# Kernel tuning notes

Hardware: AMD Instinct MI355X
Metric: run time of the kernel (lower is better)

Reference implementation:

```python
import jax, jax.numpy as jnp
import numpy as np

T, B, DIM, LATENT, OUT = 512, 1024, 128, 256, 64


def setup_inputs() -> dict:
    key = jax.random.key(0)
    ks = jax.random.split(key, 6)
    s_i = 1.0 / np.sqrt(DIM)
    s_h = 1.0 / np.sqrt(LATENT)
    return {
        "x": jax.random.normal(ks[0], (T, B, DIM), dtype=jnp.float32),
        "h": jnp.zeros((B, LATENT), dtype=jnp.float32),
        "Wi": jax.random.uniform(ks[1], (DIM, LATENT), jnp.float32, -s_i, s_i),
        "bi": jax.random.uniform(ks[2], (LATENT,), jnp.float32, -s_i, s_i),
        "Wh": jax.random.uniform(ks[3], (LATENT, LATENT), jnp.float32, -s_h, s_h),
        "Wd": jax.random.uniform(ks[4], (LATENT, OUT), jnp.float32, -s_h, s_h),
        "bd": jax.random.uniform(ks[5], (OUT,), jnp.float32, -s_h, s_h),
    }


def reference(x, h, Wi, bi, Wh, Wd, bd):
    # Precompute input projections for all steps in one big GEMM: [T,B,latent]
    xi = jnp.einsum("tbd,dl->tbl", x, Wi) + bi

    def step(h, xi_t):
        h = jnp.tanh(xi_t + h @ Wh)
        return h, None

    h_final, _ = jax.lax.scan(step, h, xi)
    return jax.nn.sigmoid(h_final @ Wd + bd)
```

## Files before the change

### kernel.cpp

```cpp
#include <hip/hip_runtime.h>
#include <cmath>
#include <cstdint>

constexpr int T_STEPS = 512;
constexpr int BATCH   = 1024;
constexpr int DIM     = 128;
constexpr int LATENT  = 256;
constexpr int OUT_DIM = 64;
constexpr int ROWS    = 16;

typedef __attribute__((ext_vector_type(8))) short bf16x8;
typedef __attribute__((ext_vector_type(4))) float f32x4;
typedef __attribute__((ext_vector_type(4))) int   i32x4;

__device__ __forceinline__ uint32_t f2bf(float f) {
    uint32_t u = __builtin_bit_cast(uint32_t, f);
    return (u + 0x7FFFu + ((u >> 16) & 1u)) >> 16;
}
__device__ __forceinline__ uint32_t pk2(float a, float b) {
    return f2bf(a) | (f2bf(b) << 16);
}
__device__ __forceinline__ float fast_tanh(float v) {
    float e = __builtin_amdgcn_exp2f(v * 2.885390081777927f);
    return __builtin_fmaf(-2.0f, __builtin_amdgcn_rcpf(e + 1.0f), 1.0f);
}
__device__ __forceinline__ float fast_sigmoid(float v) {
    float e = __builtin_amdgcn_exp2f(v * -1.4426950408889634f);
    return __builtin_amdgcn_rcpf(e + 1.0f);
}
__device__ __forceinline__ int q8(float v, float inv) {
    return (int)__builtin_rintf(v * inv);
}
__device__ __forceinline__ uint32_t pack4(int a, int b, int c, int d) {
    return (uint32_t)(a & 255) | ((uint32_t)(b & 255) << 8) |
           ((uint32_t)(c & 255) << 16) | ((uint32_t)(d & 255) << 24);
}
__device__ __forceinline__ int swz(int sl, int b) {
    return (sl ^ (b & 3) ^ ((b >> 2) & 3)) & 3;
}

__global__ __launch_bounds__(512)
void rnn_i8h(const float* __restrict__ x,
             const float* __restrict__ h0,
             const float* __restrict__ Wi,
             const float* __restrict__ bi,
             const float* __restrict__ Wh,
             const float* __restrict__ Wd,
             const float* __restrict__ bd,
             float* __restrict__ out)
{
    __shared__ __align__(16) uint8_t hls[2][4096];
    __shared__ __align__(16) uint8_t xls[2][4096];

    const int tid  = threadIdx.x;
    const int lane = tid & 63;
    const int wv   = tid >> 6;
    const int b0   = blockIdx.x * ROWS;
    const int b15  = lane & 15;
    const int kgrp = lane >> 4;
    const int tg0  = wv * 2, tg1 = wv * 2 + 1;
    const int wcol0 = tg0 * 16 + b15;
    const int wcol1 = wcol0 + 16;

    float cmh0 = 0.f, cmh1 = 0.f;
    {
        const float* p0 = Wh + (size_t)(kgrp * 16) * LATENT + wcol0;
        #pragma unroll 4
        for (int i = 0; i < 64; ++i) {
            const size_t off = (size_t)((i >> 4) * 64 + (i & 15)) * LATENT;
            cmh0 = fmaxf(cmh0, fabsf(p0[off]));
            cmh1 = fmaxf(cmh1, fabsf(p0[off + 16]));
        }
        cmh0 = fmaxf(cmh0, __shfl_xor(cmh0, 16));
        cmh0 = fmaxf(cmh0, __shfl_xor(cmh0, 32));
        cmh1 = fmaxf(cmh1, __shfl_xor(cmh1, 16));
        cmh1 = fmaxf(cmh1, __shfl_xor(cmh1, 32));
    }
    const float ih0 = cmh0 > 0.f ? 127.f / cmh0 : 0.f;
    const float ih1 = cmh1 > 0.f ? 127.f / cmh1 : 0.f;

#define WHQ(J) q8(_p[(size_t)(J) * LATENT], _inv)
#define LOADWH(NAME, WC, S, INV)                                            \
    i32x4 NAME; {                                                           \
        const float* _p = Wh + (size_t)((S) * 64 + kgrp * 16) * LATENT + (WC); \
        const float _inv = (INV);                                           \
        NAME[0] = (int)pack4(WHQ(0),  WHQ(1),  WHQ(2),  WHQ(3));            \
        NAME[1] = (int)pack4(WHQ(4),  WHQ(5),  WHQ(6),  WHQ(7));            \
        NAME[2] = (int)pack4(WHQ(8),  WHQ(9),  WHQ(10), WHQ(11));           \
        NAME[3] = (int)pack4(WHQ(12), WHQ(13), WHQ(14), WHQ(15));           \
    }
    LOADWH(AH0_0, wcol0, 0, ih0) LOADWH(AH0_1, wcol0, 1, ih0)
    LOADWH(AH0_2, wcol0, 2, ih0) LOADWH(AH0_3, wcol0, 3, ih0)
    LOADWH(AH1_0, wcol1, 0, ih1) LOADWH(AH1_1, wcol1, 1, ih1)
    LOADWH(AH1_2, wcol1, 2, ih1) LOADWH(AH1_3, wcol1, 3, ih1)

#define LOADWX(NAME, WC, S)                                                 \
    bf16x8 NAME; {                                                          \
        const float* _p = Wi + (size_t)((S) * 32 + kgrp * 8) * LATENT + (WC); \
        NAME[0] = (short)f2bf(_p[0]);                                       \
        NAME[1] = (short)f2bf(_p[(size_t)1 * LATENT]);                      \
        NAME[2] = (short)f2bf(_p[(size_t)2 * LATENT]);                      \
        NAME[3] = (short)f2bf(_p[(size_t)3 * LATENT]);                      \
        NAME[4] = (short)f2bf(_p[(size_t)4 * LATENT]);                      \
        NAME[5] = (short)f2bf(_p[(size_t)5 * LATENT]);                      \
        NAME[6] = (short)f2bf(_p[(size_t)6 * LATENT]);                      \
        NAME[7] = (short)f2bf(_p[(size_t)7 * LATENT]);                      \
    }
    LOADWX(AX0_0, wcol0, 0) LOADWX(AX0_1, wcol0, 1)
    LOADWX(AX0_2, wcol0, 2) LOADWX(AX0_3, wcol0, 3)
    LOADWX(AX1_0, wcol1, 0) LOADWX(AX1_1, wcol1, 1)
    LOADWX(AX1_2, wcol1, 2) LOADWX(AX1_3, wcol1, 3)

    const float dh0_0 = __shfl(cmh0, kgrp * 4 + 0) * (1.f / 16129.f);
    const float dh0_1 = __shfl(cmh0, kgrp * 4 + 1) * (1.f / 16129.f);
    const float dh0_2 = __shfl(cmh0, kgrp * 4 + 2) * (1.f / 16129.f);
    const float dh0_3 = __shfl(cmh0, kgrp * 4 + 3) * (1.f / 16129.f);
    const float dh1_0 = __shfl(cmh1, kgrp * 4 + 0) * (1.f / 16129.f);
    const float dh1_1 = __shfl(cmh1, kgrp * 4 + 1) * (1.f / 16129.f);
    const float dh1_2 = __shfl(cmh1, kgrp * 4 + 2) * (1.f / 16129.f);
    const float dh1_3 = __shfl(cmh1, kgrp * 4 + 3) * (1.f / 16129.f);
    const float cb0_0 = bi[tg0 * 16 + kgrp * 4 + 0];
    const float cb0_1 = bi[tg0 * 16 + kgrp * 4 + 1];
    const float cb0_2 = bi[tg0 * 16 + kgrp * 4 + 2];
    const float cb0_3 = bi[tg0 * 16 + kgrp * 4 + 3];
    const float cb1_0 = bi[tg1 * 16 + kgrp * 4 + 0];
    const float cb1_1 = bi[tg1 * 16 + kgrp * 4 + 1];
    const float cb1_2 = bi[tg1 * 16 + kgrp * 4 + 2];
    const float cb1_3 = bi[tg1 * 16 + kgrp * 4 + 3];

    const int pr = tid & 15;
    const int pq = tid >> 4;
    const int stb = (pq >> 3) * 1024 + pr * 64 +
                    (swz((pq >> 1) & 3, pr) << 4) + (pq & 1) * 8;
    {
        const float* hp = h0 + (size_t)(b0 + pr) * LATENT + pq * 8;
        uint32_t u0 = pack4(q8(hp[0], 127.f), q8(hp[1], 127.f),
                            q8(hp[2], 127.f), q8(hp[3], 127.f));
        uint32_t u1 = pack4(q8(hp[4], 127.f), q8(hp[5], 127.f),
                            q8(hp[6], 127.f), q8(hp[7], 127.f));
        *reinterpret_cast<uint2*>(&hls[0][stb]) = make_uint2(u0, u1);
        const float* xq = x + (size_t)(b0 + pr) * DIM + pq * 4;
        float4 xv = *reinterpret_cast<const float4*>(xq);
        *reinterpret_cast<uint2*>(&xls[0][stb]) =
            make_uint2(pk2(xv.x, xv.y), pk2(xv.z, xv.w));
    }
    __syncthreads();

    const int hrd = b15 * 64 + (swz(kgrp, b15) << 4);
    const int wb0 = (tg0 >> 2) * 1024 + b15 * 64 +
                    (swz(tg0 & 3, b15) << 4) + kgrp * 4;
    const int wb1 = (tg1 >> 2) * 1024 + b15 * 64 +
                    (swz(tg1 & 3, b15) << 4) + kgrp * 4;
    const float* xp = x + ((size_t)BATCH + b0 + pr) * DIM + pq * 4;

    int cur = 0;
    for (int t = 0; t < T_STEPS; ++t) {
        const bool pf = (t + 1 < T_STEPS);
        float4 xv;
        if (pf) {
            xv = *reinterpret_cast<const float4*>(xp);
            xp += (size_t)BATCH * DIM;
        }

        const uint8_t* hb = &hls[cur][hrd];
        const uint8_t* xb = &xls[cur][hrd];
        i32x4  bh0 = *reinterpret_cast<const i32x4*>(hb);
        i32x4  bh1 = *reinterpret_cast<const i32x4*>(hb + 1024);
        i32x4  bh2 = *reinterpret_cast<const i32x4*>(hb + 2048);
        i32x4  bh3 = *reinterpret_cast<const i32x4*>(hb + 3072);
        bf16x8 bx0 = *reinterpret_cast<const bf16x8*>(xb);
        bf16x8 bx1 = *reinterpret_cast<const bf16x8*>(xb + 1024);
        bf16x8 bx2 = *reinterpret_cast<const bf16x8*>(xb + 2048);
        bf16x8 bx3 = *reinterpret_cast<const bf16x8*>(xb + 3072);

        i32x4 ch0 = {0, 0, 0, 0}, ch1 = {0, 0, 0, 0};
        f32x4 cx0 = {cb0_0, cb0_1, cb0_2, cb0_3};
        f32x4 cx1 = {cb1_0, cb1_1, cb1_2, cb1_3};

        ch0 = __builtin_amdgcn_mfma_i32_16x16x64_i8(AH0_0, bh0, ch0, 0, 0, 0);
        ch1 = __builtin_amdgcn_mfma_i32_16x16x64_i8(AH1_0, bh0, ch1, 0, 0, 0);
        cx0 = __builtin_amdgcn_mfma_f32_16x16x32_bf16(AX0_0, bx0, cx0, 0, 0, 0);
        cx1 = __builtin_amdgcn_mfma_f32_16x16x32_bf16(AX1_0, bx0, cx1, 0, 0, 0);
        ch0 = __builtin_amdgcn_mfma_i32_16x16x64_i8(AH0_1, bh1, ch0, 0, 0, 0);
        ch1 = __builtin_amdgcn_mfma_i32_16x16x64_i8(AH1_1, bh1, ch1, 0, 0, 0);
        cx0 = __builtin_amdgcn_mfma_f32_16x16x32_bf16(AX0_1, bx1, cx0, 0, 0, 0);
        cx1 = __builtin_amdgcn_mfma_f32_16x16x32_bf16(AX1_1, bx1, cx1, 0, 0, 0);
        ch0 = __builtin_amdgcn_mfma_i32_16x16x64_i8(AH0_2, bh2, ch0, 0, 0, 0);
        ch1 = __builtin_amdgcn_mfma_i32_16x16x64_i8(AH1_2, bh2, ch1, 0, 0, 0);
        cx0 = __builtin_amdgcn_mfma_f32_16x16x32_bf16(AX0_2, bx2, cx0, 0, 0, 0);
        cx1 = __builtin_amdgcn_mfma_f32_16x16x32_bf16(AX1_2, bx2, cx1, 0, 0, 0);
        ch0 = __builtin_amdgcn_mfma_i32_16x16x64_i8(AH0_3, bh3, ch0, 0, 0, 0);
        ch1 = __builtin_amdgcn_mfma_i32_16x16x64_i8(AH1_3, bh3, ch1, 0, 0, 0);
        cx0 = __builtin_amdgcn_mfma_f32_16x16x32_bf16(AX0_3, bx3, cx0, 0, 0, 0);
        cx1 = __builtin_amdgcn_mfma_f32_16x16x32_bf16(AX1_3, bx3, cx1, 0, 0, 0);

        const int nxt = cur ^ 1;
        {
            float v0 = fast_tanh(__builtin_fmaf((float)ch0[0], dh0_0, cx0[0]));
            float v1 = fast_tanh(__builtin_fmaf((float)ch0[1], dh0_1, cx0[1]));
            float v2 = fast_tanh(__builtin_fmaf((float)ch0[2], dh0_2, cx0[2]));
            float v3 = fast_tanh(__builtin_fmaf((float)ch0[3], dh0_3, cx0[3]));
            *reinterpret_cast<uint32_t*>(&hls[nxt][wb0]) =
                pack4(q8(v0, 127.f), q8(v1, 127.f), q8(v2, 127.f), q8(v3, 127.f));
        }
        {
            float v0 = fast_tanh(__builtin_fmaf((float)ch1[0], dh1_0, cx1[0]));
            float v1 = fast_tanh(__builtin_fmaf((float)ch1[1], dh1_1, cx1[1]));
            float v2 = fast_tanh(__builtin_fmaf((float)ch1[2], dh1_2, cx1[2]));
            float v3 = fast_tanh(__builtin_fmaf((float)ch1[3], dh1_3, cx1[3]));
            *reinterpret_cast<uint32_t*>(&hls[nxt][wb1]) =
                pack4(q8(v0, 127.f), q8(v1, 127.f), q8(v2, 127.f), q8(v3, 127.f));
        }
        if (pf)
            *reinterpret_cast<uint2*>(&xls[nxt][stb]) =
                make_uint2(pk2(xv.x, xv.y), pk2(xv.z, xv.w));

        __syncthreads();
        cur = nxt;
    }

    {
        const int o  = tid & 63;
        const int rb = tid >> 6;
        float s0 = 0.f, s1 = 0.f;
        #pragma unroll 4
        for (int k = 0; k < LATENT; k += 4) {
            const int sl   = (k >> 4) & 3;
            const int base = (k >> 6) * 1024 + (k & 15);
            const uint32_t pA = *reinterpret_cast<const uint32_t*>(
                &hls[cur][base + rb * 64 + (swz(sl, rb) << 4)]);
            const uint32_t pB = *reinterpret_cast<const uint32_t*>(
                &hls[cur][base + (rb + 8) * 64 + (swz(sl, rb + 8) << 4)]);
            const float w0 = Wd[(size_t)(k + 0) * OUT_DIM + o];
            const float w1 = Wd[(size_t)(k + 1) * OUT_DIM + o];
            const float w2 = Wd[(size_t)(k + 2) * OUT_DIM + o];
            const float w3 = Wd[(size_t)(k + 3) * OUT_DIM + o];
            s0 += (float)(int8_t)(pA) * w0 + (float)(int8_t)(pA >> 8) * w1
                + (float)(int8_t)(pA >> 16) * w2 + (float)(int8_t)(pA >> 24) * w3;
            s1 += (float)(int8_t)(pB) * w0 + (float)(int8_t)(pB >> 8) * w1
                + (float)(int8_t)(pB >> 16) * w2 + (float)(int8_t)(pB >> 24) * w3;
        }
        out[(size_t)(b0 + rb) * OUT_DIM + o] =
            fast_sigmoid(bd[o] + s0 * (1.f / 127.f));
        out[(size_t)(b0 + rb + 8) * OUT_DIM + o] =
            fast_sigmoid(bd[o] + s1 * (1.f / 127.f));
    }
}

extern "C" void kernel_launch(void* const* d_in, const int* in_sizes, int n_in,
                              void* d_out, int out_size, void* d_ws, size_t ws_size,
                              hipStream_t stream) {
    const float* x  = (const float*)d_in[0];
    const float* h0 = (const float*)d_in[1];
    const float* Wi = (const float*)d_in[2];
    const float* bi = (const float*)d_in[3];
    const float* Wh = (const float*)d_in[4];
    const float* Wd = (const float*)d_in[5];
    const float* bd = (const float*)d_in[6];
    float* out = (float*)d_out;

    hipLaunchKernelGGL(rnn_i8h, dim3(BATCH / ROWS), dim3(512), 0, stream,
                       x, h0, Wi, bi, Wh, Wd, bd, out);
}
```

Baseline: 402.8 us.

## Split input projection into a parallel GEMM kernel ahead of recurrence

Moves the x·Wi input projection out of the sequential recurrent loop into a separate kernel that is parallel over time chunks. It writes bf16 pre-activations to workspace, and the recurrence kernel then only streams them from memory. This takes the bf16 MFMAs and the x conversion off the serial critical path. In exchange it adds a workspace round trip (about 256 MB written and then read) and a second kernel launch, and it keeps the fused kernel as a fallback when workspace is too small.

```diff
diff --git a/kernel.cpp b/kernel.cpp
--- a/kernel.cpp
+++ b/kernel.cpp
@@ -8,6 +8,7 @@
 constexpr int LATENT  = 256;
 constexpr int OUT_DIM = 64;
 constexpr int ROWS    = 16;
+constexpr int TCHUNK  = 64;
 
 typedef __attribute__((ext_vector_type(8))) short bf16x8;
 typedef __attribute__((ext_vector_type(4))) float f32x4;
@@ -17,6 +18,9 @@
     uint32_t u = __builtin_bit_cast(uint32_t, f);
     return (u + 0x7FFFu + ((u >> 16) & 1u)) >> 16;
 }
+__device__ __forceinline__ float bf2f(uint32_t b) {
+    return __builtin_bit_cast(float, b << 16);
+}
 __device__ __forceinline__ uint32_t pk2(float a, float b) {
     return f2bf(a) | (f2bf(b) << 16);
 }
@@ -38,46 +42,6 @@
 __device__ __forceinline__ int swz(int sl, int b) {
     return (sl ^ (b & 3) ^ ((b >> 2) & 3)) & 3;
 }
-
-__global__ __launch_bounds__(512)
-void rnn_i8h(const float* __restrict__ x,
-             const float* __restrict__ h0,
-             const float* __restrict__ Wi,
-             const float* __restrict__ bi,
-             const float* __restrict__ Wh,
-             const float* __restrict__ Wd,
-             const float* __restrict__ bd,
-             float* __restrict__ out)
-{
-    __shared__ __align__(16) uint8_t hls[2][4096];
-    __shared__ __align__(16) uint8_t xls[2][4096];
-
-    const int tid  = threadIdx.x;
-    const int lane = tid & 63;
-    const int wv   = tid >> 6;
-    const int b0   = blockIdx.x * ROWS;
-    const int b15  = lane & 15;
-    const int kgrp = lane >> 4;
-    const int tg0  = wv * 2, tg1 = wv * 2 + 1;
-    const int wcol0 = tg0 * 16 + b15;
-    const int wcol1 = wcol0 + 16;
-
-    float cmh0 = 0.f, cmh1 = 0.f;
-    {
-        const float* p0 = Wh + (size_t)(kgrp * 16) * LATENT + wcol0;
-        #pragma unroll 4
-        for (int i = 0; i < 64; ++i) {
-            const size_t off = (size_t)((i >> 4) * 64 + (i & 15)) * LATENT;
-            cmh0 = fmaxf(cmh0, fabsf(p0[off]));
-            cmh1 = fmaxf(cmh1, fabsf(p0[off + 16]));
-        }
-        cmh0 = fmaxf(cmh0, __shfl_xor(cmh0, 16));
-        cmh0 = fmaxf(cmh0, __shfl_xor(cmh0, 32));
-        cmh1 = fmaxf(cmh1, __shfl_xor(cmh1, 16));
-        cmh1 = fmaxf(cmh1, __shfl_xor(cmh1, 32));
-    }
-    const float ih0 = cmh0 > 0.f ? 127.f / cmh0 : 0.f;
-    const float ih1 = cmh1 > 0.f ? 127.f / cmh1 : 0.f;
 
 #define WHQ(J) q8(_p[(size_t)(J) * LATENT], _inv)
 #define LOADWH(NAME, WC, S, INV)                                            \
@@ -89,11 +53,6 @@
         NAME[2] = (int)pack4(WHQ(8),  WHQ(9),  WHQ(10), WHQ(11));           \
         NAME[3] = (int)pack4(WHQ(12), WHQ(13), WHQ(14), WHQ(15));           \
     }
-    LOADWH(AH0_0, wcol0, 0, ih0) LOADWH(AH0_1, wcol0, 1, ih0)
-    LOADWH(AH0_2, wcol0, 2, ih0) LOADWH(AH0_3, wcol0, 3, ih0)
-    LOADWH(AH1_0, wcol1, 0, ih1) LOADWH(AH1_1, wcol1, 1, ih1)
-    LOADWH(AH1_2, wcol1, 2, ih1) LOADWH(AH1_3, wcol1, 3, ih1)
-
 #define LOADWX(NAME, WC, S)                                                 \
     bf16x8 NAME; {                                                          \
         const float* _p = Wi + (size_t)((S) * 32 + kgrp * 8) * LATENT + (WC); \
@@ -106,10 +65,137 @@
         NAME[6] = (short)f2bf(_p[(size_t)6 * LATENT]);                      \
         NAME[7] = (short)f2bf(_p[(size_t)7 * LATENT]);                      \
     }
+
+__global__ __launch_bounds__(512)
+void rnn_xi_gemm(const float* __restrict__ x,
+                 const float* __restrict__ Wi,
+                 const float* __restrict__ bi,
+                 uint2* __restrict__ xi)
+{
+    __shared__ __align__(16) uint8_t xls[2][4096];
+
+    const int tid  = threadIdx.x;
+    const int lane = tid & 63;
+    const int wv   = tid >> 6;
+    const int blk  = blockIdx.x;
+    const int t0   = blockIdx.y * TCHUNK;
+    const int b0   = blk * ROWS;
+    const int b15  = lane & 15;
+    const int kgrp = lane >> 4;
+    const int tg0  = wv * 2, tg1 = wv * 2 + 1;
+    const int wcol0 = tg0 * 16 + b15;
+    const int wcol1 = wcol0 + 16;
+
     LOADWX(AX0_0, wcol0, 0) LOADWX(AX0_1, wcol0, 1)
     LOADWX(AX0_2, wcol0, 2) LOADWX(AX0_3, wcol0, 3)
     LOADWX(AX1_0, wcol1, 0) LOADWX(AX1_1, wcol1, 1)
     LOADWX(AX1_2, wcol1, 2) LOADWX(AX1_3, wcol1, 3)
+
+    const float cb0_0 = bi[tg0 * 16 + kgrp * 4 + 0];
+    const float cb0_1 = bi[tg0 * 16 + kgrp * 4 + 1];
+    const float cb0_2 = bi[tg0 * 16 + kgrp * 4 + 2];
+    const float cb0_3 = bi[tg0 * 16 + kgrp * 4 + 3];
+    const float cb1_0 = bi[tg1 * 16 + kgrp * 4 + 0];
+    const float cb1_1 = bi[tg1 * 16 + kgrp * 4 + 1];
+    const float cb1_2 = bi[tg1 * 16 + kgrp * 4 + 2];
+    const float cb1_3 = bi[tg1 * 16 + kgrp * 4 + 3];
+
+    const int pr = tid & 15;
+    const int pq = tid >> 4;
+    const int stb = (pq >> 3) * 1024 + pr * 64 +
+                    (swz((pq >> 1) & 3, pr) << 4) + (pq & 1) * 8;
+    {
+        const float* xq = x + ((size_t)t0 * BATCH + b0 + pr) * DIM + pq * 4;
+        float4 xv = *reinterpret_cast<const float4*>(xq);
+        *reinterpret_cast<uint2*>(&xls[0][stb]) =
+            make_uint2(pk2(xv.x, xv.y), pk2(xv.z, xv.w));
+    }
+    __syncthreads();
+
+    const int hrd = b15 * 64 + (swz(kgrp, b15) << 4);
+    const float* xp = x + ((size_t)(t0 + 1) * BATCH + b0 + pr) * DIM + pq * 4;
+    uint2* wp = xi + ((((size_t)t0 * 64 + blk) << 10) + (wv << 7) + lane);
+
+    int cur = 0;
+    for (int tt = 0; tt < TCHUNK; ++tt) {
+        const bool pf = (tt + 1 < TCHUNK);
+        float4 xv;
+        if (pf) {
+            xv = *reinterpret_cast<const float4*>(xp);
+            xp += (size_t)BATCH * DIM;
+        }
+
+        const uint8_t* xb = &xls[cur][hrd];
+        bf16x8 bx0 = *reinterpret_cast<const bf16x8*>(xb);
+        bf16x8 bx1 = *reinterpret_cast<const bf16x8*>(xb + 1024);
+        bf16x8 bx2 = *reinterpret_cast<const bf16x8*>(xb + 2048);
+        bf16x8 bx3 = *reinterpret_cast<const bf16x8*>(xb + 3072);
+
+        f32x4 c0 = {cb0_0, cb0_1, cb0_2, cb0_3};
+        f32x4 c1 = {cb1_0, cb1_1, cb1_2, cb1_3};
+        c0 = __builtin_amdgcn_mfma_f32_16x16x32_bf16(AX0_0, bx0, c0, 0, 0, 0);
+        c1 = __builtin_amdgcn_mfma_f32_16x16x32_bf16(AX1_0, bx0, c1, 0, 0, 0);
+        c0 = __builtin_amdgcn_mfma_f32_16x16x32_bf16(AX0_1, bx1, c0, 0, 0, 0);
+        c1 = __builtin_amdgcn_mfma_f32_16x16x32_bf16(AX1_1, bx1, c1, 0, 0, 0);
+        c0 = __builtin_amdgcn_mfma_f32_16x16x32_bf16(AX0_2, bx2, c0, 0, 0, 0);
+        c1 = __builtin_amdgcn_mfma_f32_16x16x32_bf16(AX1_2, bx2, c1, 0, 0, 0);
+        c0 = __builtin_amdgcn_mfma_f32_16x16x32_bf16(AX0_3, bx3, c0, 0, 0, 0);
+        c1 = __builtin_amdgcn_mfma_f32_16x16x32_bf16(AX1_3, bx3, c1, 0, 0, 0);
+
+        wp[0]  = make_uint2(pk2(c0[0], c0[1]), pk2(c0[2], c0[3]));
+        wp[64] = make_uint2(pk2(c1[0], c1[1]), pk2(c1[2], c1[3]));
+        wp += 65536;
+
+        if (pf)
+            *reinterpret_cast<uint2*>(&xls[cur ^ 1][stb]) =
+                make_uint2(pk2(xv.x, xv.y), pk2(xv.z, xv.w));
+        __syncthreads();
+        cur ^= 1;
+    }
+}
+
+__global__ __launch_bounds__(512)
+void rnn_rec(const float* __restrict__ h0,
+             const float* __restrict__ Wh,
+             const float* __restrict__ Wd,
+             const float* __restrict__ bd,
+             const uint2* __restrict__ xi,
+             float* __restrict__ out)
+{
+    __shared__ __align__(16) uint8_t hls[2][4096];
+
+    const int tid  = threadIdx.x;
+    const int lane = tid & 63;
+    const int wv   = tid >> 6;
+    const int blk  = blockIdx.x;
+    const int b0   = blk * ROWS;
+    const int b15  = lane & 15;
+    const int kgrp = lane >> 4;
+    const int tg0  = wv * 2, tg1 = wv * 2 + 1;
+    const int wcol0 = tg0 * 16 + b15;
+    const int wcol1 = wcol0 + 16;
+
+    float cmh0 = 0.f, cmh1 = 0.f;
+    {
+        const float* p0 = Wh + (size_t)(kgrp * 16) * LATENT + wcol0;
+        #pragma unroll 4
+        for (int i = 0; i < 64; ++i) {
+            const size_t off = (size_t)((i >> 4) * 64 + (i & 15)) * LATENT;
+            cmh0 = fmaxf(cmh0, fabsf(p0[off]));
+            cmh1 = fmaxf(cmh1, fabsf(p0[off + 16]));
+        }
+        cmh0 = fmaxf(cmh0, __shfl_xor(cmh0, 16));
+        cmh0 = fmaxf(cmh0, __shfl_xor(cmh0, 32));
+        cmh1 = fmaxf(cmh1, __shfl_xor(cmh1, 16));
+        cmh1 = fmaxf(cmh1, __shfl_xor(cmh1, 32));
+    }
+    const float ih0 = cmh0 > 0.f ? 127.f / cmh0 : 0.f;
+    const float ih1 = cmh1 > 0.f ? 127.f / cmh1 : 0.f;
+
+    LOADWH(AH0_0, wcol0, 0, ih0) LOADWH(AH0_1, wcol0, 1, ih0)
+    LOADWH(AH0_2, wcol0, 2, ih0) LOADWH(AH0_3, wcol0, 3, ih0)
+    LOADWH(AH1_0, wcol1, 0, ih1) LOADWH(AH1_1, wcol1, 1, ih1)
+    LOADWH(AH1_2, wcol1, 2, ih1) LOADWH(AH1_3, wcol1, 3, ih1)
 
     const float dh0_0 = __shfl(cmh0, kgrp * 4 + 0) * (1.f / 16129.f);
     const float dh0_1 = __shfl(cmh0, kgrp * 4 + 1) * (1.f / 16129.f);
@@ -119,14 +205,6 @@
     const float dh1_1 = __shfl(cmh1, kgrp * 4 + 1) * (1.f / 16129.f);
     const float dh1_2 = __shfl(cmh1, kgrp * 4 + 2) * (1.f / 16129.f);
     const float dh1_3 = __shfl(cmh1, kgrp * 4 + 3) * (1.f / 16129.f);
-    const float cb0_0 = bi[tg0 * 16 + kgrp * 4 + 0];
-    const float cb0_1 = bi[tg0 * 16 + kgrp * 4 + 1];
-    const float cb0_2 = bi[tg0 * 16 + kgrp * 4 + 2];
-    const float cb0_3 = bi[tg0 * 16 + kgrp * 4 + 3];
-    const float cb1_0 = bi[tg1 * 16 + kgrp * 4 + 0];
-    const float cb1_1 = bi[tg1 * 16 + kgrp * 4 + 1];
-    const float cb1_2 = bi[tg1 * 16 + kgrp * 4 + 2];
-    const float cb1_3 = bi[tg1 * 16 + kgrp * 4 + 3];
 
     const int pr = tid & 15;
     const int pq = tid >> 4;
@@ -139,10 +217,6 @@
         uint32_t u1 = pack4(q8(hp[4], 127.f), q8(hp[5], 127.f),
                             q8(hp[6], 127.f), q8(hp[7], 127.f));
         *reinterpret_cast<uint2*>(&hls[0][stb]) = make_uint2(u0, u1);
-        const float* xq = x + (size_t)(b0 + pr) * DIM + pq * 4;
-        float4 xv = *reinterpret_cast<const float4*>(xq);
-        *reinterpret_cast<uint2*>(&xls[0][stb]) =
-            make_uint2(pk2(xv.x, xv.y), pk2(xv.z, xv.w));
     }
     __syncthreads();
 
@@ -151,70 +225,56 @@
                     (swz(tg0 & 3, b15) << 4) + kgrp * 4;
     const int wb1 = (tg1 >> 2) * 1024 + b15 * 64 +
                     (swz(tg1 & 3, b15) << 4) + kgrp * 4;
-    const float* xp = x + ((size_t)BATCH + b0 + pr) * DIM + pq * 4;
+
+    const uint2* xr = xi + ((size_t)blk << 10) + (wv << 7) + lane;
+    uint2 xa0 = xr[0];
+    uint2 xa1 = xr[64];
 
     int cur = 0;
     for (int t = 0; t < T_STEPS; ++t) {
         const bool pf = (t + 1 < T_STEPS);
-        float4 xv;
+        uint2 xb0, xb1;
         if (pf) {
-            xv = *reinterpret_cast<const float4*>(xp);
-            xp += (size_t)BATCH * DIM;
+            xb0 = xr[65536];
+            xb1 = xr[65536 + 64];
         }
 
         const uint8_t* hb = &hls[cur][hrd];
-        const uint8_t* xb = &xls[cur][hrd];
-        i32x4  bh0 = *reinterpret_cast<const i32x4*>(hb);
-        i32x4  bh1 = *reinterpret_cast<const i32x4*>(hb + 1024);
-        i32x4  bh2 = *reinterpret_cast<const i32x4*>(hb + 2048);
-        i32x4  bh3 = *reinterpret_cast<const i32x4*>(hb + 3072);
-        bf16x8 bx0 = *reinterpret_cast<const bf16x8*>(xb);
-        bf16x8 bx1 = *reinterpret_cast<const bf16x8*>(xb + 1024);
-        bf16x8 bx2 = *reinterpret_cast<const bf16x8*>(xb + 2048);
-        bf16x8 bx3 = *reinterpret_cast<const bf16x8*>(xb + 3072);
+        i32x4 bh0 = *reinterpret_cast<const i32x4*>(hb);
+        i32x4 bh1 = *reinterpret_cast<const i32x4*>(hb + 1024);
+        i32x4 bh2 = *reinterpret_cast<const i32x4*>(hb + 2048);
+        i32x4 bh3 = *reinterpret_cast<const i32x4*>(hb + 3072);
 
         i32x4 ch0 = {0, 0, 0, 0}, ch1 = {0, 0, 0, 0};
-        f32x4 cx0 = {cb0_0, cb0_1, cb0_2, cb0_3};
-        f32x4 cx1 = {cb1_0, cb1_1, cb1_2, cb1_3};
-
         ch0 = __builtin_amdgcn_mfma_i32_16x16x64_i8(AH0_0, bh0, ch0, 0, 0, 0);
         ch1 = __builtin_amdgcn_mfma_i32_16x16x64_i8(AH1_0, bh0, ch1, 0, 0, 0);
-        cx0 = __builtin_amdgcn_mfma_f32_16x16x32_bf16(AX0_0, bx0, cx0, 0, 0, 0);
-        cx1 = __builtin_amdgcn_mfma_f32_16x16x32_bf16(AX1_0, bx0, cx1, 0, 0, 0);
         ch0 = __builtin_amdgcn_mfma_i32_16x16x64_i8(AH0_1, bh1, ch0, 0, 0, 0);
         ch1 = __builtin_amdgcn_mfma_i32_16x16x64_i8(AH1_1, bh1, ch1, 0, 0, 0);
-        cx0 = __builtin_amdgcn_mfma_f32_16x16x32_bf16(AX0_1, bx1, cx0, 0, 0, 0);
-        cx1 = __builtin_amdgcn_mfma_f32_16x16x32_bf16(AX1_1, bx1, cx1, 0, 0, 0);
         ch0 = __builtin_amdgcn_mfma_i32_16x16x64_i8(AH0_2, bh2, ch0, 0, 0, 0);
         ch1 = __builtin_amdgcn_mfma_i32_16x16x64_i8(AH1_2, bh2, ch1, 0, 0, 0);
-        cx0 = __builtin_amdgcn_mfma_f32_16x16x32_bf16(AX0_2, bx2, cx0, 0, 0, 0);
-        cx1 = __builtin_amdgcn_mfma_f32_16x16x32_bf16(AX1_2, bx2, cx1, 0, 0, 0);
         ch0 = __builtin_amdgcn_mfma_i32_16x16x64_i8(AH0_3, bh3, ch0, 0, 0, 0);
         ch1 = __builtin_amdgcn_mfma_i32_16x16x64_i8(AH1_3, bh3, ch1, 0, 0, 0);
-        cx0 = __builtin_amdgcn_mfma_f32_16x16x32_bf16(AX0_3, bx3, cx0, 0, 0, 0);
-        cx1 = __builtin_amdgcn_mfma_f32_16x16x32_bf16(AX1_3, bx3, cx1, 0, 0, 0);
 
         const int nxt = cur ^ 1;
         {
-            float v0 = fast_tanh(__builtin_fmaf((float)ch0[0], dh0_0, cx0[0]));
-            float v1 = fast_tanh(__builtin_fmaf((float)ch0[1], dh0_1, cx0[1]));
-            float v2 = fast_tanh(__builtin_fmaf((float)ch0[2], dh0_2, cx0[2]));
-            float v3 = fast_tanh(__builtin_fmaf((float)ch0[3], dh0_3, cx0[3]));
+            float v0 = fast_tanh(__builtin_fmaf((float)ch0[0], dh0_0, bf2f(xa0.x & 0xFFFFu)));
+            float v1 = fast_tanh(__builtin_fmaf((float)ch0[1], dh0_1, bf2f(xa0.x >> 16)));
+            float v2 = fast_tanh(__builtin_fmaf((float)ch0[2], dh0_2, bf2f(xa0.y & 0xFFFFu)));
+            float v3 = fast_tanh(__builtin_fmaf((float)ch0[3], dh0_3, bf2f(xa0.y >> 16)));
             *reinterpret_cast<uint32_t*>(&hls[nxt][wb0]) =
                 pack4(q8(v0, 127.f), q8(v1, 127.f), q8(v2, 127.f), q8(v3, 127.f));
         }
         {
-            float v0 = fast_tanh(__builtin_fmaf((float)ch1[0], dh1_0, cx1[0]));
-            float v1 = fast_tanh(__builtin_fmaf((float)ch1[1], dh1_1, cx1[1]));
-            float v2 = fast_tanh(__builtin_fmaf((float)ch1[2], dh1_2, cx1[2]));
-            float v3 = fast_tanh(__builtin_fmaf((float)ch1[3], dh1_3, cx1[3]));
+            float v0 = fast_tanh(__builtin_fmaf((float)ch1[0], dh1_0, bf2f(xa1.x & 0xFFFFu)));
+            float v1 = fast_tanh(__builtin_fmaf((float)ch1[1], dh1_1, bf2f(xa1.x >> 16)));
+            float v2 = fast_tanh(__builtin_fmaf((float)ch1[2], dh1_2, bf2f(xa1.y & 0xFFFFu)));
+            float v3 = fast_tanh(__builtin_fmaf((float)ch1[3], dh1_3, bf2f(xa1.y >> 16)));
             *reinterpret_cast<uint32_t*>(&hls[nxt][wb1]) =
                 pack4(q8(v0, 127.f), q8(v1, 127.f), q8(v2, 127.f), q8(v3, 127.f));
         }
-        if (pf)
-            *reinterpret_cast<uint2*>(&xls[nxt][stb]) =
-                make_uint2(pk2(xv.x, xv.y), pk2(xv.z, xv.w));
-
+
+        if (pf) { xa0 = xb0; xa1 = xb1; }
+        xr += 65536;
         __syncthreads();
         cur = nxt;
     }
@@ -247,6 +307,184 @@
     }
 }
 
+__global__ __launch_bounds__(512)
+void rnn_i8h(const float* __restrict__ x, const float* __restrict__ h0,
+             const float* __restrict__ Wi, const float* __restrict__ bi,
+             const float* __restrict__ Wh, const float* __restrict__ Wd,
+             const float* __restrict__ bd, float* __restrict__ out)
+{
+    __shared__ __align__(16) uint8_t hls[2][4096];
+    __shared__ __align__(16) uint8_t xls[2][4096];
+
+    const int tid  = threadIdx.x;
+    const int lane = tid & 63;
+    const int wv   = tid >> 6;
+    const int b0   = blockIdx.x * ROWS;
+    const int b15  = lane & 15;
+    const int kgrp = lane >> 4;
+    const int tg0  = wv * 2, tg1 = wv * 2 + 1;
+    const int wcol0 = tg0 * 16 + b15;
+    const int wcol1 = wcol0 + 16;
+
+    float cmh0 = 0.f, cmh1 = 0.f;
+    {
+        const float* p0 = Wh + (size_t)(kgrp * 16) * LATENT + wcol0;
+        #pragma unroll 4
+        for (int i = 0; i < 64; ++i) {
+            const size_t off = (size_t)((i >> 4) * 64 + (i & 15)) * LATENT;
+            cmh0 = fmaxf(cmh0, fabsf(p0[off]));
+            cmh1 = fmaxf(cmh1, fabsf(p0[off + 16]));
+        }
+        cmh0 = fmaxf(cmh0, __shfl_xor(cmh0, 16));
+        cmh0 = fmaxf(cmh0, __shfl_xor(cmh0, 32));
+        cmh1 = fmaxf(cmh1, __shfl_xor(cmh1, 16));
+        cmh1 = fmaxf(cmh1, __shfl_xor(cmh1, 32));
+    }
+    const float ih0 = cmh0 > 0.f ? 127.f / cmh0 : 0.f;
+    const float ih1 = cmh1 > 0.f ? 127.f / cmh1 : 0.f;
+
+    LOADWH(FH0_0, wcol0, 0, ih0) LOADWH(FH0_1, wcol0, 1, ih0)
+    LOADWH(FH0_2, wcol0, 2, ih0) LOADWH(FH0_3, wcol0, 3, ih0)
+    LOADWH(FH1_0, wcol1, 0, ih1) LOADWH(FH1_1, wcol1, 1, ih1)
+    LOADWH(FH1_2, wcol1, 2, ih1) LOADWH(FH1_3, wcol1, 3, ih1)
+    LOADWX(FX0_0, wcol0, 0) LOADWX(FX0_1, wcol0, 1)
+    LOADWX(FX0_2, wcol0, 2) LOADWX(FX0_3, wcol0, 3)
+    LOADWX(FX1_0, wcol1, 0) LOADWX(FX1_1, wcol1, 1)
+    LOADWX(FX1_2, wcol1, 2) LOADWX(FX1_3, wcol1, 3)
+
+    const float dh0_0 = __shfl(cmh0, kgrp * 4 + 0) * (1.f / 16129.f);
+    const float dh0_1 = __shfl(cmh0, kgrp * 4 + 1) * (1.f / 16129.f);
+    const float dh0_2 = __shfl(cmh0, kgrp * 4 + 2) * (1.f / 16129.f);
+    const float dh0_3 = __shfl(cmh0, kgrp * 4 + 3) * (1.f / 16129.f);
+    const float dh1_0 = __shfl(cmh1, kgrp * 4 + 0) * (1.f / 16129.f);
+    const float dh1_1 = __shfl(cmh1, kgrp * 4 + 1) * (1.f / 16129.f);
+    const float dh1_2 = __shfl(cmh1, kgrp * 4 + 2) * (1.f / 16129.f);
+    const float dh1_3 = __shfl(cmh1, kgrp * 4 + 3) * (1.f / 16129.f);
+    const float cb0_0 = bi[tg0 * 16 + kgrp * 4 + 0];
+    const float cb0_1 = bi[tg0 * 16 + kgrp * 4 + 1];
+    const float cb0_2 = bi[tg0 * 16 + kgrp * 4 + 2];
+    const float cb0_3 = bi[tg0 * 16 + kgrp * 4 + 3];
+    const float cb1_0 = bi[tg1 * 16 + kgrp * 4 + 0];
+    const float cb1_1 = bi[tg1 * 16 + kgrp * 4 + 1];
+    const float cb1_2 = bi[tg1 * 16 + kgrp * 4 + 2];
+    const float cb1_3 = bi[tg1 * 16 + kgrp * 4 + 3];
+
+    const int pr = tid & 15;
+    const int pq = tid >> 4;
+    const int stb = (pq >> 3) * 1024 + pr * 64 +
+                    (swz((pq >> 1) & 3, pr) << 4) + (pq & 1) * 8;
+    {
+        const float* hp = h0 + (size_t)(b0 + pr) * LATENT + pq * 8;
+        uint32_t u0 = pack4(q8(hp[0], 127.f), q8(hp[1], 127.f),
+                            q8(hp[2], 127.f), q8(hp[3], 127.f));
+        uint32_t u1 = pack4(q8(hp[4], 127.f), q8(hp[5], 127.f),
+                            q8(hp[6], 127.f), q8(hp[7], 127.f));
+        *reinterpret_cast<uint2*>(&hls[0][stb]) = make_uint2(u0, u1);
+        const float* xq = x + (size_t)(b0 + pr) * DIM + pq * 4;
+        float4 xv = *reinterpret_cast<const float4*>(xq);
+        *reinterpret_cast<uint2*>(&xls[0][stb]) =
+            make_uint2(pk2(xv.x, xv.y), pk2(xv.z, xv.w));
+    }
+    __syncthreads();
+
+    const int hrd = b15 * 64 + (swz(kgrp, b15) << 4);
+    const int wb0 = (tg0 >> 2) * 1024 + b15 * 64 +
+                    (swz(tg0 & 3, b15) << 4) + kgrp * 4;
+    const int wb1 = (tg1 >> 2) * 1024 + b15 * 64 +
+                    (swz(tg1 & 3, b15) << 4) + kgrp * 4;
+    const float* xp = x + ((size_t)BATCH + b0 + pr) * DIM + pq * 4;
+
+    int cur = 0;
+    for (int t = 0; t < T_STEPS; ++t) {
+        const bool pf = (t + 1 < T_STEPS);
+        float4 xv;
+        if (pf) {
+            xv = *reinterpret_cast<const float4*>(xp);
+            xp += (size_t)BATCH * DIM;
+        }
+        const uint8_t* hb = &hls[cur][hrd];
+        const uint8_t* xb = &xls[cur][hrd];
+        i32x4  bh0 = *reinterpret_cast<const i32x4*>(hb);
+        i32x4  bh1 = *reinterpret_cast<const i32x4*>(hb + 1024);
+        i32x4  bh2 = *reinterpret_cast<const i32x4*>(hb + 2048);
+        i32x4  bh3 = *reinterpret_cast<const i32x4*>(hb + 3072);
+        bf16x8 bx0 = *reinterpret_cast<const bf16x8*>(xb);
+        bf16x8 bx1 = *reinterpret_cast<const bf16x8*>(xb + 1024);
+        bf16x8 bx2 = *reinterpret_cast<const bf16x8*>(xb + 2048);
+        bf16x8 bx3 = *reinterpret_cast<const bf16x8*>(xb + 3072);
+
+        i32x4 ch0 = {0, 0, 0, 0}, ch1 = {0, 0, 0, 0};
+        f32x4 cx0 = {cb0_0, cb0_1, cb0_2, cb0_3};
+        f32x4 cx1 = {cb1_0, cb1_1, cb1_2, cb1_3};
+        ch0 = __builtin_amdgcn_mfma_i32_16x16x64_i8(FH0_0, bh0, ch0, 0, 0, 0);
+        ch1 = __builtin_amdgcn_mfma_i32_16x16x64_i8(FH1_0, bh0, ch1, 0, 0, 0);
+        cx0 = __builtin_amdgcn_mfma_f32_16x16x32_bf16(FX0_0, bx0, cx0, 0, 0, 0);
+        cx1 = __builtin_amdgcn_mfma_f32_16x16x32_bf16(FX1_0, bx0, cx1, 0, 0, 0);
+        ch0 = __builtin_amdgcn_mfma_i32_16x16x64_i8(FH0_1, bh1, ch0, 0, 0, 0);
+        ch1 = __builtin_amdgcn_mfma_i32_16x16x64_i8(FH1_1, bh1, ch1, 0, 0, 0);
+        cx0 = __builtin_amdgcn_mfma_f32_16x16x32_bf16(FX0_1, bx1, cx0, 0, 0, 0);
+        cx1 = __builtin_amdgcn_mfma_f32_16x16x32_bf16(FX1_1, bx1, cx1, 0, 0, 0);
+        ch0 = __builtin_amdgcn_mfma_i32_16x16x64_i8(FH0_2, bh2, ch0, 0, 0, 0);
+        ch1 = __builtin_amdgcn_mfma_i32_16x16x64_i8(FH1_2, bh2, ch1, 0, 0, 0);
+        cx0 = __builtin_amdgcn_mfma_f32_16x16x32_bf16(FX0_2, bx2, cx0, 0, 0, 0);
+        cx1 = __builtin_amdgcn_mfma_f32_16x16x32_bf16(FX1_2, bx2, cx1, 0, 0, 0);
+        ch0 = __builtin_amdgcn_mfma_i32_16x16x64_i8(FH0_3, bh3, ch0, 0, 0, 0);
+        ch1 = __builtin_amdgcn_mfma_i32_16x16x64_i8(FH1_3, bh3, ch1, 0, 0, 0);
+        cx0 = __builtin_amdgcn_mfma_f32_16x16x32_bf16(FX0_3, bx3, cx0, 0, 0, 0);
+        cx1 = __builtin_amdgcn_mfma_f32_16x16x32_bf16(FX1_3, bx3, cx1, 0, 0, 0);
+
+        const int nxt = cur ^ 1;
+        {
+            float v0 = fast_tanh(__builtin_fmaf((float)ch0[0], dh0_0, cx0[0]));
+            float v1 = fast_tanh(__builtin_fmaf((float)ch0[1], dh0_1, cx0[1]));
+            float v2 = fast_tanh(__builtin_fmaf((float)ch0[2], dh0_2, cx0[2]));
+            float v3 = fast_tanh(__builtin_fmaf((float)ch0[3], dh0_3, cx0[3]));
+            *reinterpret_cast<uint32_t*>(&hls[nxt][wb0]) =
+                pack4(q8(v0, 127.f), q8(v1, 127.f), q8(v2, 127.f), q8(v3, 127.f));
+        }
+        {
+            float v0 = fast_tanh(__builtin_fmaf((float)ch1[0], dh1_0, cx1[0]));
+            float v1 = fast_tanh(__builtin_fmaf((float)ch1[1], dh1_1, cx1[1]));
+            float v2 = fast_tanh(__builtin_fmaf((float)ch1[2], dh1_2, cx1[2]));
+            float v3 = fast_tanh(__builtin_fmaf((float)ch1[3], dh1_3, cx1[3]));
+            *reinterpret_cast<uint32_t*>(&hls[nxt][wb1]) =
+                pack4(q8(v0, 127.f), q8(v1, 127.f), q8(v2, 127.f), q8(v3, 127.f));
+        }
+        if (pf)
+            *reinterpret_cast<uint2*>(&xls[nxt][stb]) =
+                make_uint2(pk2(xv.x, xv.y), pk2(xv.z, xv.w));
+        __syncthreads();
+        cur = nxt;
+    }
+
+    {
+        const int o  = tid & 63;
+        const int rb = tid >> 6;
+        float s0 = 0.f, s1 = 0.f;
+        #pragma unroll 4
+        for (int k = 0; k < LATENT; k += 4) {
+            const int sl   = (k >> 4) & 3;
+            const int base = (k >> 6) * 1024 + (k & 15);
+            const uint32_t pA = *reinterpret_cast<const uint32_t*>(
+                &hls[cur][base + rb * 64 + (swz(sl, rb) << 4)]);
+            const uint32_t pB = *reinterpret_cast<const uint32_t*>(
+                &hls[cur][base + (rb + 8) * 64 + (swz(sl, rb + 8) << 4)]);
+            const float w0 = Wd[(size_t)(k + 0) * OUT_DIM + o];
+            const float w1 = Wd[(size_t)(k + 1) * OUT_DIM + o];
+            const float w2 = Wd[(size_t)(k + 2) * OUT_DIM + o];
+            const float w3 = Wd[(size_t)(k + 3) * OUT_DIM + o];
+            s0 += (float)(int8_t)(pA) * w0 + (float)(int8_t)(pA >> 8) * w1
+                + (float)(int8_t)(pA >> 16) * w2 + (float)(int8_t)(pA >> 24) * w3;
+            s1 += (float)(int8_t)(pB) * w0 + (float)(int8_t)(pB >> 8) * w1
+                + (float)(int8_t)(pB >> 16) * w2 + (float)(int8_t)(pB >> 24) * w3;
+        }
+        out[(size_t)(b0 + rb) * OUT_DIM + o] =
+            fast_sigmoid(bd[o] + s0 * (1.f / 127.f));
+        out[(size_t)(b0 + rb + 8) * OUT_DIM + o] =
+            fast_sigmoid(bd[o] + s1 * (1.f / 127.f));
+    }
+}
+
 extern "C" void kernel_launch(void* const* d_in, const int* in_sizes, int n_in,
                               void* d_out, int out_size, void* d_ws, size_t ws_size,
                               hipStream_t stream) {
@@ -259,6 +497,14 @@
     const float* bd = (const float*)d_in[6];
     float* out = (float*)d_out;
 
-    hipLaunchKernelGGL(rnn_i8h, dim3(BATCH / ROWS), dim3(512), 0, stream,
-                       x, h0, Wi, bi, Wh, Wd, bd, out);
-}
+    const size_t need = (size_t)T_STEPS * 64 * 1024 * sizeof(uint2);
+    if (ws_size >= need) {
+        hipLaunchKernelGGL(rnn_xi_gemm, dim3(64, T_STEPS / TCHUNK), dim3(512),
+                           0, stream, x, Wi, bi, (uint2*)d_ws);
+        hipLaunchKernelGGL(rnn_rec, dim3(64), dim3(512), 0, stream,
+                           h0, Wh, Wd, bd, (const uint2*)d_ws, out);
+    } else {
+        hipLaunchKernelGGL(rnn_i8h, dim3(BATCH / ROWS), dim3(512), 0, stream,
+                           x, h0, Wi, bi, Wh, Wd, bd, out);
+    }
+}
```

Measured after the change: 430.4 us. 6.9% more time.
